# Performance work log

Hardware: AMD Instinct MI355X
Metric: run time of the kernel (lower is better)

The kernel has to match this reference:

```python
import jax, jax.numpy as jnp
import numpy as np

N_HEADS = 16

def setup_inputs() -> dict:
    key = jax.random.key(0)
    ks = jax.random.split(key, 5)
    D = 1024
    B, T = 4, 1024
    scale = 1.0 / np.sqrt(D)
    x = jax.random.normal(ks[0], (B, T, D), dtype=jnp.float32)
    Wq = jax.random.normal(ks[1], (D, D), dtype=jnp.float32) * scale
    Wk = jax.random.normal(ks[2], (D, D), dtype=jnp.float32) * scale
    Wv = jax.random.normal(ks[3], (D, D), dtype=jnp.float32) * scale
    Wo = jax.random.normal(ks[4], (D, D), dtype=jnp.float32) * scale
    return {"x": x, "Wq": Wq, "Wk": Wk, "Wv": Wv, "Wo": Wo}


def reference(x, Wq, Wk, Wv, Wo):
    # FLA BasedLinearAttention (mode='chunk', normalize=True, scale=1) with
    # Taylor feature map phi(u) = [1, u/d^{1/4}, (u (x) u)/sqrt(2 d)], so
    # phi(q)·phi(k) = 1 + s + s^2/2 where s = (q·k)/sqrt(d).
    B, T, D = x.shape
    H = N_HEADS
    d = D // H  # head_dim == feature_dim
    # torch Linear: y = x @ W.T (bias=False in FLA proj layers)
    q = (x @ Wq.T).reshape(B, T, H, d).transpose(0, 2, 1, 3)  # b h t d
    k = (x @ Wk.T).reshape(B, T, H, d).transpose(0, 2, 1, 3)
    v = (x @ Wv.T).reshape(B, T, H, d).transpose(0, 2, 1, 3)
    s = jnp.einsum('bhtd,bhsd->bhts', q, k) / jnp.sqrt(jnp.float32(d))
    scores = 1.0 + s + 0.5 * s * s  # always > 0 (= ((s+1)^2+1)/2)
    causal = jnp.tril(jnp.ones((T, T), dtype=bool))
    scores = jnp.where(causal, scores, 0.0)
    num = jnp.einsum('bhts,bhsd->bhtd', scores, v)
    den = jnp.sum(scores, axis=-1, keepdims=True)
    o = num / den  # b h t d
    o = o.transpose(0, 2, 1, 3).reshape(B, T, D)  # b t (h d)
    return o @ Wo.T
```

## Files before the change

### kernel.cpp

```cpp
#include <hip/hip_runtime.h>

typedef unsigned short u16;
typedef __attribute__((ext_vector_type(8))) short bf16x8;
typedef __attribute__((ext_vector_type(8))) unsigned short u16x8;
typedef __attribute__((ext_vector_type(4))) float f32x4;

#define MFMA16(a, b, c) __builtin_amdgcn_mfma_f32_16x16x32_bf16((a), (b), (c), 0, 0, 0)

__device__ __forceinline__ void gll16(const void* g, void* l) {
    __builtin_amdgcn_global_load_lds(
        (const __attribute__((address_space(1))) unsigned int*)g,
        (__attribute__((address_space(3))) unsigned int*)l, 16, 0, 0);
}

__device__ __forceinline__ u16 f2b(float f) {
    unsigned int u = __float_as_uint(f);
    u += 0x7fffu + ((u >> 16) & 1u);
    return (u16)(u >> 16);
}

__device__ __forceinline__ unsigned int pkcvt(float a, float b) {
    unsigned int r;
    asm("v_cvt_pk_bf16_f32 %0, %1, %2" : "=v"(r) : "v"(a), "v"(b));
    return r;
}

__global__ __launch_bounds__(256) void cast_all(const float* __restrict__ x,
                                                const float* __restrict__ w0,
                                                const float* __restrict__ w1,
                                                const float* __restrict__ w2,
                                                const float* __restrict__ w3,
                                                u16* __restrict__ xb,
                                                u16* __restrict__ wb) {
    const int bid = blockIdx.x;
    const float* s; u16* d; int off;
    if (bid < 2048) { s = x; d = xb; off = bid; }
    else {
        const int wi = (bid - 2048) >> 9;
        s = (wi == 0) ? w0 : (wi == 1) ? w1 : (wi == 2) ? w2 : w3;
        d = wb + (size_t)wi * 1048576;
        off = (bid - 2048) & 511;
    }
    const int i = (off * 256 + threadIdx.x) * 8;
    float4 a = *(const float4*)(s + i);
    float4 b = *(const float4*)(s + i + 4);
    *(uint4*)(d + i) = make_uint4(pkcvt(a.x, a.y), pkcvt(a.z, a.w),
                                  pkcvt(b.x, b.y), pkcvt(b.z, b.w));
}

template <int BM, int BN, int MODE, int SLOTS>
__global__ __launch_bounds__(256) void gemm_bt(const u16* __restrict__ A,
                                               const u16* __restrict__ W,
                                               void* __restrict__ Yv,
                                               u16* __restrict__ vT,
                                               int K, int ldY) {
    constexpr int MI = BM / 32, NJ = BN / 32;
    constexpr int ACH = BM / 16;
    constexpr int NPW = (BM + BN) / 64;
    __shared__ u16 As[2][SLOTS][BM * 32];
    __shared__ u16 Bs[2][SLOTS][BN * 32];
    const int t = threadIdx.x, w = t >> 6, lane = t & 63;
    const int quad = lane >> 4, m16 = lane & 15;
    const int wr = (w >> 1) * (BM / 2), wc = (w & 1) * (BN / 2);
    const int row0 = blockIdx.x * BM, col0 = blockIdx.y * BN;
    const int srow = lane >> 2, scol = (lane & 3) * 8;

    auto stage = [&](int buf, int slot, int k0) {
#pragma unroll
        for (int cc = 0; cc < NPW; ++cc) {
            const int c = w * NPW + cc;
            if (c < ACH)
                gll16(A + (size_t)(row0 + c * 16 + srow) * K + k0 + scol,
                      &As[buf][slot][c * 512]);
            else
                gll16(W + (size_t)(col0 + (c - ACH) * 16 + srow) * K + k0 + scol,
                      &Bs[buf][slot][(c - ACH) * 512]);
        }
    };

    f32x4 acc[MI][NJ];
#pragma unroll
    for (int i = 0; i < MI; ++i)
#pragma unroll
        for (int j = 0; j < NJ; ++j) acc[i][j] = (f32x4){0.f, 0.f, 0.f, 0.f};

    auto compute_tile = [&](int buf, int slot) {
        bf16x8 af[MI], bf[NJ];
#pragma unroll
        for (int i = 0; i < MI; ++i)
            af[i] = *(const bf16x8*)&As[buf][slot][(wr + i * 16 + m16) * 32 + quad * 8];
#pragma unroll
        for (int j = 0; j < NJ; ++j)
            bf[j] = *(const bf16x8*)&Bs[buf][slot][(wc + j * 16 + m16) * 32 + quad * 8];
#pragma unroll
        for (int i = 0; i < MI; ++i)
#pragma unroll
            for (int j = 0; j < NJ; ++j) acc[i][j] = MFMA16(af[i], bf[j], acc[i][j]);
    };

#pragma unroll
    for (int s = 0; s < SLOTS; ++s) stage(0, s, s * 32);
    const int ngroups = K / (32 * SLOTS);
    for (int g = 0; g < ngroups; ++g) {
        const int buf = g & 1;
        __syncthreads();
        const int kn = (g + 1) * SLOTS * 32;
        if (kn < K) {
#pragma unroll
            for (int s = 0; s < SLOTS; ++s) stage(buf ^ 1, s, kn + s * 32);
        }
#pragma unroll
        for (int s = 0; s < SLOTS; ++s) compute_tile(buf, s);
    }
    if constexpr (MODE == 0) {
#pragma unroll
        for (int i = 0; i < MI; ++i)
#pragma unroll
            for (int j = 0; j < NJ; ++j)
#pragma unroll
                for (int r = 0; r < 4; ++r)
                    ((float*)Yv)[(size_t)(row0 + wr + i * 16 + quad * 4 + r) * ldY +
                                 col0 + wc + j * 16 + m16] = acc[i][j][r];
    } else {
        if (col0 < 2048) {
            u16* qk = (u16*)Yv;
#pragma unroll
            for (int i = 0; i < MI; ++i)
#pragma unroll
                for (int j = 0; j < NJ; ++j)
#pragma unroll
                    for (int r = 0; r < 4; ++r)
                        qk[(size_t)(row0 + wr + i * 16 + quad * 4 + r) * 2048 +
                           col0 + wc + j * 16 + m16] = f2b(acc[i][j][r]);
        } else {
#pragma unroll
            for (int i = 0; i < MI; ++i) {
                const int rbase = row0 + wr + i * 16;
                const int bb = rbase >> 10;
                const int tok0 = (rbase & 1023) + quad * 4;
#pragma unroll
                for (int j = 0; j < NJ; ++j) {
                    const int vTrow = bb * 1024 + (col0 + wc + j * 16 + m16 - 2048);
                    *(uint2*)(vT + (size_t)vTrow * 1024 + tok0) =
                        make_uint2(pkcvt(acc[i][j][0], acc[i][j][1]),
                                   pkcvt(acc[i][j][2], acc[i][j][3]));
                }
            }
        }
    }
}

__global__ __launch_bounds__(256) void based_attn(const u16* __restrict__ qkm,
                                                  const u16* __restrict__ vT,
                                                  u16* __restrict__ o) {
    __shared__ u16 ks[2][2][64][32];
    __shared__ u16 vs[2][2][64][32];
    __shared__ u16 SsA[2][64][32];
    __shared__ u16 SsB[2][64][32];

    const int t = threadIdx.x, w = t >> 6, lane = t & 63;
    const int quad = lane >> 4, m16 = lane & 15;
    const int p = blockIdx.x, h = blockIdx.y, b = blockIdx.z;
    const int tA = p, tB = 15 - p;
    const int srow = lane >> 2, s8 = (lane & 3) * 8;
    const int qrow = w * 16 + m16;

    const size_t qbase = (size_t)b * 1024 * 2048 + h * 64;
    const size_t kbase = qbase + 1024;
    const size_t vbase = ((size_t)b * 1024 + h * 64) * 1024;

    bf16x8 qfA[2], qfB[2];
#pragma unroll
    for (int kd = 0; kd < 2; ++kd) {
        qfA[kd] = *(const bf16x8*)(qkm + qbase +
                   (size_t)(tA * 64 + qrow) * 2048 + kd * 32 + quad * 8);
        qfB[kd] = *(const bf16x8*)(qkm + qbase +
                   (size_t)(tB * 64 + qrow) * 2048 + kd * 32 + quad * 8);
    }

    auto stage_tile = [&](int kt, int buf) {
#pragma unroll
        for (int cc = 0; cc < 2; ++cc) {
            const int c = w * 2 + cc;
            const int blk = c >> 2, rc = c & 3;
            gll16(qkm + kbase + (size_t)(kt * 64 + rc * 16 + srow) * 2048 + blk * 32 + s8,
                  &ks[buf][blk][rc * 16][0]);
            gll16(vT + vbase + (size_t)(rc * 16 + srow) * 1024 + kt * 64 + blk * 32 + s8,
                  &vs[buf][blk][rc * 16][0]);
        }
    };

    bf16x8 ones;
#pragma unroll
    for (int e = 0; e < 8; ++e) ones[e] = (short)0x3F80;

    f32x4 numA[4], numB[4], denA, denB;
    denA = denB = (f32x4){0.f, 0.f, 0.f, 0.f};
#pragma unroll
    for (int j = 0; j < 4; ++j) numA[j] = numB[j] = (f32x4){0.f, 0.f, 0.f, 0.f};

    auto compute = [&](int buf, int kt) {
        const bool doA = (kt <= tA);
        f32x4 sA[4], sB[4];
#pragma unroll
        for (int jk = 0; jk < 4; ++jk)
            sA[jk] = sB[jk] = (f32x4){0.f, 0.f, 0.f, 0.f};
        __builtin_amdgcn_s_setprio(1);
#pragma unroll
        for (int kd = 0; kd < 2; ++kd)
#pragma unroll
            for (int jk = 0; jk < 4; ++jk) {
                bf16x8 af = *(const bf16x8*)&ks[buf][kd][jk * 16 + m16][quad * 8];
                sB[jk] = MFMA16(af, qfB[kd], sB[jk]);
                if (doA) sA[jk] = MFMA16(af, qfA[kd], sA[jk]);
            }
        __builtin_amdgcn_s_setprio(0);
#pragma unroll
        for (int jk = 0; jk < 4; ++jk) {
            const int kl = jk * 16 + quad * 4;
            float scB[4];
#pragma unroll
            for (int r = 0; r < 4; ++r) {
                const float u = fmaf(sB[jk][r], 0.125f, 1.0f);
                scB[r] = fmaf(u * 0.5f, u, 0.5f);
            }
            if (kt == tB) {
#pragma unroll
                for (int r = 0; r < 4; ++r)
                    if (kl + r > qrow) scB[r] = 0.f;
            }
            *(uint2*)&SsB[kl >> 5][qrow][kl & 31] =
                make_uint2(pkcvt(scB[0], scB[1]), pkcvt(scB[2], scB[3]));
            if (doA) {
                float scA[4];
#pragma unroll
                for (int r = 0; r < 4; ++r) {
                    const float u = fmaf(sA[jk][r], 0.125f, 1.0f);
                    scA[r] = fmaf(u * 0.5f, u, 0.5f);
                }
                if (kt == tA) {
#pragma unroll
                    for (int r = 0; r < 4; ++r)
                        if (kl + r > qrow) scA[r] = 0.f;
                }
                *(uint2*)&SsA[kl >> 5][qrow][kl & 31] =
                    make_uint2(pkcvt(scA[0], scA[1]), pkcvt(scA[2], scA[3]));
            }
        }
        __builtin_amdgcn_s_setprio(1);
#pragma unroll
        for (int kb = 0; kb < 2; ++kb) {
            bf16x8 vf[4];
#pragma unroll
            for (int j = 0; j < 4; ++j)
                vf[j] = *(const bf16x8*)&vs[buf][kb][j * 16 + m16][quad * 8];
            bf16x8 sfB = *(const bf16x8*)&SsB[kb][qrow][quad * 8];
#pragma unroll
            for (int j = 0; j < 4; ++j) numB[j] = MFMA16(sfB, vf[j], numB[j]);
            denB = MFMA16(sfB, ones, denB);
            if (doA) {
                bf16x8 sfA = *(const bf16x8*)&SsA[kb][qrow][quad * 8];
#pragma unroll
                for (int j = 0; j < 4; ++j) numA[j] = MFMA16(sfA, vf[j], numA[j]);
                denA = MFMA16(sfA, ones, denA);
            }
        }
        __builtin_amdgcn_s_setprio(0);
    };

    stage_tile(0, 0);
    for (int kt = 0; kt <= tB; ++kt) {
        const int buf = kt & 1;
        __syncthreads();
        if (kt + 1 <= tB) stage_tile(kt + 1, buf ^ 1);
        compute(buf, kt);
    }

#pragma unroll
    for (int r = 0; r < 4; ++r) {
        const float invA = 1.0f / denA[r], invB = 1.0f / denB[r];
        const int rowoff = w * 16 + quad * 4 + r;
        const size_t tokA = (size_t)(b * 1024 + tA * 64 + rowoff);
        const size_t tokB = (size_t)(b * 1024 + tB * 64 + rowoff);
#pragma unroll
        for (int j = 0; j < 4; ++j) {
            o[tokA * 1024 + h * 64 + j * 16 + m16] = f2b(numA[j][r] * invA);
            o[tokB * 1024 + h * 64 + j * 16 + m16] = f2b(numB[j][r] * invB);
        }
    }
}

extern "C" void kernel_launch(void* const* d_in, const int* in_sizes, int n_in,
                              void* d_out, int out_size, void* d_ws, size_t ws_size,
                              hipStream_t stream) {
    const float* x  = (const float*)d_in[0];
    const float* Wq = (const float*)d_in[1];
    const float* Wk = (const float*)d_in[2];
    const float* Wv = (const float*)d_in[3];
    const float* Wo = (const float*)d_in[4];
    float* out = (float*)d_out;

    const size_t MEL = 4096ull * 1024ull;
    u16* xb   = (u16*)d_ws;
    u16* Wqkv = xb + MEL;
    u16* Wob  = Wqkv + 3ull * 1024 * 1024;
    u16* qk   = Wob + 1024ull * 1024;
    u16* vT   = qk + 2ull * MEL;
    u16* o    = vT + MEL;

    cast_all<<<4096, 256, 0, stream>>>(x, Wq, Wk, Wv, Wo, xb, Wqkv);

    dim3 gq(32, 24);
    gemm_bt<128, 128, 1, 1><<<gq, 256, 0, stream>>>(xb, Wqkv, qk, vT, 1024, 2048);

    dim3 ga(8, 16, 4);
    based_attn<<<ga, 256, 0, stream>>>(qk, vT, o);

    dim3 go(32, 16);
    gemm_bt<128, 64, 0, 2><<<go, 256, 0, stream>>>(o, Wob, (void*)out, nullptr, 1024, 1024);
}
```

Baseline: 160.9 us.

## Rewrite attention kernel with 32x32 MFMA and register-resident score matrix

Reworks the based-attention kernel so each wave owns a 32-row query strip and uses 32x32x16 bf16 MFMAs for both QK^T and score·V. The score tile is no longer round-tripped through shared memory. It is converted to bf16 in registers and the halves are exchanged across the wave with shuffles to form the A operand. Query strips are assigned per wave in a balanced causal pattern (p, 31-p, 8+p, 23-p). Waves with shorter strips skip compute while still taking part in the shared K/V staging and barriers. This removes LDS writes and reads of the scores and lowers MFMA instruction count. The cost is more register pressure and intra-block imbalance, since the block runs to the longest strip.

New measurement: 182.3 us. 1.13x slower.

```diff
diff --git a/kernel.cpp b/kernel.cpp
--- a/kernel.cpp
+++ b/kernel.cpp
@@ -2,10 +2,11 @@
 
 typedef unsigned short u16;
 typedef __attribute__((ext_vector_type(8))) short bf16x8;
-typedef __attribute__((ext_vector_type(8))) unsigned short u16x8;
 typedef __attribute__((ext_vector_type(4))) float f32x4;
+typedef __attribute__((ext_vector_type(16))) float f32x16;
 
 #define MFMA16(a, b, c) __builtin_amdgcn_mfma_f32_16x16x32_bf16((a), (b), (c), 0, 0, 0)
+#define MFMA32(a, b, c) __builtin_amdgcn_mfma_f32_32x32x16_bf16((a), (b), (c), 0, 0, 0)
 
 __device__ __forceinline__ void gll16(const void* g, void* l) {
     __builtin_amdgcn_global_load_lds(
@@ -150,33 +151,29 @@
     }
 }
 
-__global__ __launch_bounds__(256) void based_attn(const u16* __restrict__ qkm,
-                                                  const u16* __restrict__ vT,
-                                                  u16* __restrict__ o) {
+__global__ __launch_bounds__(256) void based_attn32(const u16* __restrict__ qkm,
+                                                    const u16* __restrict__ vT,
+                                                    u16* __restrict__ o) {
     __shared__ u16 ks[2][2][64][32];
     __shared__ u16 vs[2][2][64][32];
-    __shared__ u16 SsA[2][64][32];
-    __shared__ u16 SsB[2][64][32];
 
     const int t = threadIdx.x, w = t >> 6, lane = t & 63;
-    const int quad = lane >> 4, m16 = lane & 15;
-    const int p = blockIdx.x, h = blockIdx.y, b = blockIdx.z;
-    const int tA = p, tB = 15 - p;
+    const int m = lane & 31, h = lane >> 5;
+    const int p = blockIdx.x, hh = blockIdx.y, b = blockIdx.z;
+    const int j = (w == 0) ? p : (w == 1) ? (31 - p) : (w == 2) ? (8 + p) : (23 - p);
+    const int ktmax_w = j >> 1;
+    const int KTMAX = (31 - p) >> 1;
     const int srow = lane >> 2, s8 = (lane & 3) * 8;
-    const int qrow = w * 16 + m16;
-
-    const size_t qbase = (size_t)b * 1024 * 2048 + h * 64;
+
+    const size_t qbase = (size_t)b * 1024 * 2048 + hh * 64;
     const size_t kbase = qbase + 1024;
-    const size_t vbase = ((size_t)b * 1024 + h * 64) * 1024;
-
-    bf16x8 qfA[2], qfB[2];
-#pragma unroll
-    for (int kd = 0; kd < 2; ++kd) {
-        qfA[kd] = *(const bf16x8*)(qkm + qbase +
-                   (size_t)(tA * 64 + qrow) * 2048 + kd * 32 + quad * 8);
-        qfB[kd] = *(const bf16x8*)(qkm + qbase +
-                   (size_t)(tB * 64 + qrow) * 2048 + kd * 32 + quad * 8);
-    }
+    const size_t vbase = ((size_t)b * 1024 + hh * 64) * 1024;
+
+    bf16x8 qf[4];
+#pragma unroll
+    for (int kd = 0; kd < 4; ++kd)
+        qf[kd] = *(const bf16x8*)(qkm + qbase + (size_t)(j * 32 + m) * 2048 +
+                                  kd * 16 + h * 8);
 
     auto stage_tile = [&](int kt, int buf) {
 #pragma unroll
@@ -194,99 +191,95 @@
 #pragma unroll
     for (int e = 0; e < 8; ++e) ones[e] = (short)0x3F80;
 
-    f32x4 numA[4], numB[4], denA, denB;
-    denA = denB = (f32x4){0.f, 0.f, 0.f, 0.f};
-#pragma unroll
-    for (int j = 0; j < 4; ++j) numA[j] = numB[j] = (f32x4){0.f, 0.f, 0.f, 0.f};
+    f32x16 num0, num1, den;
+#pragma unroll
+    for (int e = 0; e < 16; ++e) { num0[e] = 0.f; num1[e] = 0.f; den[e] = 0.f; }
 
     auto compute = [&](int buf, int kt) {
-        const bool doA = (kt <= tA);
-        f32x4 sA[4], sB[4];
-#pragma unroll
-        for (int jk = 0; jk < 4; ++jk)
-            sA[jk] = sB[jk] = (f32x4){0.f, 0.f, 0.f, 0.f};
-        __builtin_amdgcn_s_setprio(1);
-#pragma unroll
-        for (int kd = 0; kd < 2; ++kd)
-#pragma unroll
-            for (int jk = 0; jk < 4; ++jk) {
-                bf16x8 af = *(const bf16x8*)&ks[buf][kd][jk * 16 + m16][quad * 8];
-                sB[jk] = MFMA16(af, qfB[kd], sB[jk]);
-                if (doA) sA[jk] = MFMA16(af, qfA[kd], sA[jk]);
+        const bool diag = (kt == ktmax_w);
+        const bool odd = (j & 1) != 0;
+        const bool do1 = (!diag) || odd;
+
+        f32x16 s0, s1;
+#pragma unroll
+        for (int e = 0; e < 16; ++e) { s0[e] = 0.f; s1[e] = 0.f; }
+#pragma unroll
+        for (int kd = 0; kd < 4; ++kd) {
+            bf16x8 k0 = *(const bf16x8*)&ks[buf][kd >> 1][m][(kd & 1) * 16 + h * 8];
+            s0 = MFMA32(k0, qf[kd], s0);
+            if (do1) {
+                bf16x8 k1 = *(const bf16x8*)&ks[buf][kd >> 1][32 + m][(kd & 1) * 16 + h * 8];
+                s1 = MFMA32(k1, qf[kd], s1);
             }
-        __builtin_amdgcn_s_setprio(0);
-#pragma unroll
-        for (int jk = 0; jk < 4; ++jk) {
-            const int kl = jk * 16 + quad * 4;
-            float scB[4];
-#pragma unroll
-            for (int r = 0; r < 4; ++r) {
-                const float u = fmaf(sB[jk][r], 0.125f, 1.0f);
-                scB[r] = fmaf(u * 0.5f, u, 0.5f);
+        }
+
+        float sc0[16], sc1[16];
+#pragma unroll
+        for (int r = 0; r < 16; ++r) {
+            const int kl = (r & 3) + 8 * (r >> 2) + 4 * h;
+            float u0 = fmaf(s0[r], 0.125f, 1.0f);
+            float v0 = fmaf(u0 * 0.5f, u0, 0.5f);
+            if (diag && !odd && kl > m) v0 = 0.f;
+            sc0[r] = v0;
+            float v1 = 0.f;
+            if (do1) {
+                float u1 = fmaf(s1[r], 0.125f, 1.0f);
+                v1 = fmaf(u1 * 0.5f, u1, 0.5f);
+                if (diag && odd && kl > m) v1 = 0.f;
             }
-            if (kt == tB) {
-#pragma unroll
-                for (int r = 0; r < 4; ++r)
-                    if (kl + r > qrow) scB[r] = 0.f;
+            sc1[r] = v1;
+        }
+
+        unsigned o0[8], o1[8], p0[8], p1[8];
+#pragma unroll
+        for (int i = 0; i < 8; ++i) {
+            o0[i] = pkcvt(sc0[2 * i], sc0[2 * i + 1]);
+            o1[i] = pkcvt(sc1[2 * i], sc1[2 * i + 1]);
+        }
+#pragma unroll
+        for (int i = 0; i < 8; ++i) {
+            p0[i] = __shfl_xor(o0[i], 32);
+            p1[i] = __shfl_xor(o1[i], 32);
+        }
+
+#pragma unroll
+        for (int ksi = 0; ksi < 4; ++ksi) {
+            const int bx = (ksi & 1) * 4 + 2 * h;
+            union { unsigned u[4]; bf16x8 v; } af;
+            if (ksi < 2) {
+                af.u[0] = h ? p0[bx] : o0[bx];
+                af.u[1] = h ? p0[bx + 1] : o0[bx + 1];
+                af.u[2] = h ? o0[bx] : p0[bx];
+                af.u[3] = h ? o0[bx + 1] : p0[bx + 1];
+            } else {
+                af.u[0] = h ? p1[bx] : o1[bx];
+                af.u[1] = h ? p1[bx + 1] : o1[bx + 1];
+                af.u[2] = h ? o1[bx] : p1[bx];
+                af.u[3] = h ? o1[bx + 1] : p1[bx + 1];
             }
-            *(uint2*)&SsB[kl >> 5][qrow][kl & 31] =
-                make_uint2(pkcvt(scB[0], scB[1]), pkcvt(scB[2], scB[3]));
-            if (doA) {
-                float scA[4];
-#pragma unroll
-                for (int r = 0; r < 4; ++r) {
-                    const float u = fmaf(sA[jk][r], 0.125f, 1.0f);
-                    scA[r] = fmaf(u * 0.5f, u, 0.5f);
-                }
-                if (kt == tA) {
-#pragma unroll
-                    for (int r = 0; r < 4; ++r)
-                        if (kl + r > qrow) scA[r] = 0.f;
-                }
-                *(uint2*)&SsA[kl >> 5][qrow][kl & 31] =
-                    make_uint2(pkcvt(scA[0], scA[1]), pkcvt(scA[2], scA[3]));
-            }
-        }
-        __builtin_amdgcn_s_setprio(1);
-#pragma unroll
-        for (int kb = 0; kb < 2; ++kb) {
-            bf16x8 vf[4];
-#pragma unroll
-            for (int j = 0; j < 4; ++j)
-                vf[j] = *(const bf16x8*)&vs[buf][kb][j * 16 + m16][quad * 8];
-            bf16x8 sfB = *(const bf16x8*)&SsB[kb][qrow][quad * 8];
-#pragma unroll
-            for (int j = 0; j < 4; ++j) numB[j] = MFMA16(sfB, vf[j], numB[j]);
-            denB = MFMA16(sfB, ones, denB);
-            if (doA) {
-                bf16x8 sfA = *(const bf16x8*)&SsA[kb][qrow][quad * 8];
-#pragma unroll
-                for (int j = 0; j < 4; ++j) numA[j] = MFMA16(sfA, vf[j], numA[j]);
-                denA = MFMA16(sfA, ones, denA);
-            }
-        }
-        __builtin_amdgcn_s_setprio(0);
+            bf16x8 v0 = *(const bf16x8*)&vs[buf][ksi >> 1][m][(ksi & 1) * 16 + h * 8];
+            bf16x8 v1 = *(const bf16x8*)&vs[buf][ksi >> 1][32 + m][(ksi & 1) * 16 + h * 8];
+            num0 = MFMA32(af.v, v0, num0);
+            num1 = MFMA32(af.v, v1, num1);
+            den  = MFMA32(af.v, ones, den);
+        }
     };
 
     stage_tile(0, 0);
-    for (int kt = 0; kt <= tB; ++kt) {
+    for (int kt = 0; kt <= KTMAX; ++kt) {
         const int buf = kt & 1;
         __syncthreads();
-        if (kt + 1 <= tB) stage_tile(kt + 1, buf ^ 1);
-        compute(buf, kt);
-    }
-
-#pragma unroll
-    for (int r = 0; r < 4; ++r) {
-        const float invA = 1.0f / denA[r], invB = 1.0f / denB[r];
-        const int rowoff = w * 16 + quad * 4 + r;
-        const size_t tokA = (size_t)(b * 1024 + tA * 64 + rowoff);
-        const size_t tokB = (size_t)(b * 1024 + tB * 64 + rowoff);
-#pragma unroll
-        for (int j = 0; j < 4; ++j) {
-            o[tokA * 1024 + h * 64 + j * 16 + m16] = f2b(numA[j][r] * invA);
-            o[tokB * 1024 + h * 64 + j * 16 + m16] = f2b(numB[j][r] * invB);
-        }
+        if (kt < KTMAX) stage_tile(kt + 1, buf ^ 1);
+        if (kt <= ktmax_w) compute(buf, kt);
+    }
+
+#pragma unroll
+    for (int r = 0; r < 16; ++r) {
+        const int q = (r & 3) + 8 * (r >> 2) + 4 * h;
+        const float inv = 1.0f / den[r];
+        const size_t tok = (size_t)(b * 1024 + j * 32 + q);
+        o[tok * 1024 + hh * 64 + m]      = f2b(num0[r] * inv);
+        o[tok * 1024 + hh * 64 + 32 + m] = f2b(num1[r] * inv);
     }
 }
 
@@ -314,7 +307,7 @@
     gemm_bt<128, 128, 1, 1><<<gq, 256, 0, stream>>>(xb, Wqkv, qk, vT, 1024, 2048);
 
     dim3 ga(8, 16, 4);
-    based_attn<<<ga, 256, 0, stream>>>(qk, vT, o);
+    based_attn32<<<ga, 256, 0, stream>>>(qk, vT, o);
 
     dim3 go(32, 16);
     gemm_bt<128, 64, 0, 2><<<go, 256, 0, stream>>>(o, Wob, (void*)out, nullptr, 1024, 1024);
```

## Keep attention scores in registers and use one query tile per block

Applied to the files above, without the earlier changes.

The attention kernel no longer writes the score tile to shared memory and reads it back. It computes S transposed (K·Q), packs the scores into bf16 register fragments, and feeds them straight into 16x16x16 MFMAs against V read from LDS. The denominator becomes a scalar row sum with a cross-lane shuffle instead of an extra MFMA against a ones vector. The grid goes from paired query tiles (p, 15-p) per block to one query tile per block, which doubles the block count but loses the pairing's load balance and its sharing of K/V staging between two tiles.

Result: slower. 204.6 us (+27.2%).

```diff
diff --git a/kernel.cpp b/kernel.cpp
--- a/kernel.cpp
+++ b/kernel.cpp
@@ -2,10 +2,20 @@
 
 typedef unsigned short u16;
 typedef __attribute__((ext_vector_type(8))) short bf16x8;
-typedef __attribute__((ext_vector_type(8))) unsigned short u16x8;
+typedef __attribute__((ext_vector_type(4))) short s16x4;
+typedef __attribute__((ext_vector_type(2))) int i32x2;
 typedef __attribute__((ext_vector_type(4))) float f32x4;
 
 #define MFMA16(a, b, c) __builtin_amdgcn_mfma_f32_16x16x32_bf16((a), (b), (c), 0, 0, 0)
+
+__device__ __forceinline__ void mfma161616(i32x2 a, i32x2 b, f32x4& c) {
+#if __has_builtin(__builtin_amdgcn_mfma_f32_16x16x16bf16_1k)
+    union { i32x2 i; s16x4 s; } ua{a}, ub{b};
+    c = __builtin_amdgcn_mfma_f32_16x16x16bf16_1k(ua.s, ub.s, c, 0, 0, 0);
+#else
+    asm("v_mfma_f32_16x16x16_bf16 %0, %1, %2, %0" : "+v"(c) : "v"(a), "v"(b));
+#endif
+}
 
 __device__ __forceinline__ void gll16(const void* g, void* l) {
     __builtin_amdgcn_global_load_lds(
@@ -155,13 +165,10 @@
                                                   u16* __restrict__ o) {
     __shared__ u16 ks[2][2][64][32];
     __shared__ u16 vs[2][2][64][32];
-    __shared__ u16 SsA[2][64][32];
-    __shared__ u16 SsB[2][64][32];
 
     const int t = threadIdx.x, w = t >> 6, lane = t & 63;
     const int quad = lane >> 4, m16 = lane & 15;
-    const int p = blockIdx.x, h = blockIdx.y, b = blockIdx.z;
-    const int tA = p, tB = 15 - p;
+    const int tq = blockIdx.x, h = blockIdx.y, b = blockIdx.z;
     const int srow = lane >> 2, s8 = (lane & 3) * 8;
     const int qrow = w * 16 + m16;
 
@@ -169,14 +176,11 @@
     const size_t kbase = qbase + 1024;
     const size_t vbase = ((size_t)b * 1024 + h * 64) * 1024;
 
-    bf16x8 qfA[2], qfB[2];
-#pragma unroll
-    for (int kd = 0; kd < 2; ++kd) {
-        qfA[kd] = *(const bf16x8*)(qkm + qbase +
-                   (size_t)(tA * 64 + qrow) * 2048 + kd * 32 + quad * 8);
-        qfB[kd] = *(const bf16x8*)(qkm + qbase +
-                   (size_t)(tB * 64 + qrow) * 2048 + kd * 32 + quad * 8);
-    }
+    bf16x8 qf[2];
+#pragma unroll
+    for (int kd = 0; kd < 2; ++kd)
+        qf[kd] = *(const bf16x8*)(qkm + qbase +
+                  (size_t)(tq * 64 + qrow) * 2048 + kd * 32 + quad * 8);
 
     auto stage_tile = [&](int kt, int buf) {
 #pragma unroll
@@ -190,104 +194,72 @@
         }
     };
 
-    bf16x8 ones;
-#pragma unroll
-    for (int e = 0; e < 8; ++e) ones[e] = (short)0x3F80;
-
-    f32x4 numA[4], numB[4], denA, denB;
-    denA = denB = (f32x4){0.f, 0.f, 0.f, 0.f};
-#pragma unroll
-    for (int j = 0; j < 4; ++j) numA[j] = numB[j] = (f32x4){0.f, 0.f, 0.f, 0.f};
+    f32x4 num[4];
+    float dens = 0.f;
+#pragma unroll
+    for (int j = 0; j < 4; ++j) num[j] = (f32x4){0.f, 0.f, 0.f, 0.f};
 
     auto compute = [&](int buf, int kt) {
-        const bool doA = (kt <= tA);
-        f32x4 sA[4], sB[4];
-#pragma unroll
-        for (int jk = 0; jk < 4; ++jk)
-            sA[jk] = sB[jk] = (f32x4){0.f, 0.f, 0.f, 0.f};
+        f32x4 s[4];
+#pragma unroll
+        for (int jk = 0; jk < 4; ++jk) s[jk] = (f32x4){0.f, 0.f, 0.f, 0.f};
         __builtin_amdgcn_s_setprio(1);
 #pragma unroll
         for (int kd = 0; kd < 2; ++kd)
 #pragma unroll
             for (int jk = 0; jk < 4; ++jk) {
                 bf16x8 af = *(const bf16x8*)&ks[buf][kd][jk * 16 + m16][quad * 8];
-                sB[jk] = MFMA16(af, qfB[kd], sB[jk]);
-                if (doA) sA[jk] = MFMA16(af, qfA[kd], sA[jk]);
+                s[jk] = MFMA16(af, qf[kd], s[jk]);
             }
         __builtin_amdgcn_s_setprio(0);
+        i32x2 sb[4];
 #pragma unroll
         for (int jk = 0; jk < 4; ++jk) {
             const int kl = jk * 16 + quad * 4;
-            float scB[4];
+            float sc[4];
 #pragma unroll
             for (int r = 0; r < 4; ++r) {
-                const float u = fmaf(sB[jk][r], 0.125f, 1.0f);
-                scB[r] = fmaf(u * 0.5f, u, 0.5f);
-            }
-            if (kt == tB) {
+                const float u = fmaf(s[jk][r], 0.125f, 1.0f);
+                sc[r] = fmaf(u * 0.5f, u, 0.5f);
+            }
+            if (kt == tq) {
 #pragma unroll
                 for (int r = 0; r < 4; ++r)
-                    if (kl + r > qrow) scB[r] = 0.f;
-            }
-            *(uint2*)&SsB[kl >> 5][qrow][kl & 31] =
-                make_uint2(pkcvt(scB[0], scB[1]), pkcvt(scB[2], scB[3]));
-            if (doA) {
-                float scA[4];
-#pragma unroll
-                for (int r = 0; r < 4; ++r) {
-                    const float u = fmaf(sA[jk][r], 0.125f, 1.0f);
-                    scA[r] = fmaf(u * 0.5f, u, 0.5f);
-                }
-                if (kt == tA) {
-#pragma unroll
-                    for (int r = 0; r < 4; ++r)
-                        if (kl + r > qrow) scA[r] = 0.f;
-                }
-                *(uint2*)&SsA[kl >> 5][qrow][kl & 31] =
-                    make_uint2(pkcvt(scA[0], scA[1]), pkcvt(scA[2], scA[3]));
-            }
+                    if (kl + r > qrow) sc[r] = 0.f;
+            }
+            dens += sc[0] + sc[1] + sc[2] + sc[3];
+            sb[jk][0] = (int)pkcvt(sc[0], sc[1]);
+            sb[jk][1] = (int)pkcvt(sc[2], sc[3]);
         }
         __builtin_amdgcn_s_setprio(1);
 #pragma unroll
-        for (int kb = 0; kb < 2; ++kb) {
-            bf16x8 vf[4];
-#pragma unroll
-            for (int j = 0; j < 4; ++j)
-                vf[j] = *(const bf16x8*)&vs[buf][kb][j * 16 + m16][quad * 8];
-            bf16x8 sfB = *(const bf16x8*)&SsB[kb][qrow][quad * 8];
-#pragma unroll
-            for (int j = 0; j < 4; ++j) numB[j] = MFMA16(sfB, vf[j], numB[j]);
-            denB = MFMA16(sfB, ones, denB);
-            if (doA) {
-                bf16x8 sfA = *(const bf16x8*)&SsA[kb][qrow][quad * 8];
-#pragma unroll
-                for (int j = 0; j < 4; ++j) numA[j] = MFMA16(sfA, vf[j], numA[j]);
-                denA = MFMA16(sfA, ones, denA);
+        for (int jk = 0; jk < 4; ++jk) {
+            const int kb = jk >> 1, ko = (jk & 1) * 16 + quad * 4;
+#pragma unroll
+            for (int j = 0; j < 4; ++j) {
+                i32x2 va = *(const i32x2*)&vs[buf][kb][j * 16 + m16][ko];
+                mfma161616(va, sb[jk], num[j]);
             }
         }
         __builtin_amdgcn_s_setprio(0);
     };
 
     stage_tile(0, 0);
-    for (int kt = 0; kt <= tB; ++kt) {
+    for (int kt = 0; kt <= tq; ++kt) {
         const int buf = kt & 1;
         __syncthreads();
-        if (kt + 1 <= tB) stage_tile(kt + 1, buf ^ 1);
+        if (kt < tq) stage_tile(kt + 1, buf ^ 1);
         compute(buf, kt);
     }
 
-#pragma unroll
-    for (int r = 0; r < 4; ++r) {
-        const float invA = 1.0f / denA[r], invB = 1.0f / denB[r];
-        const int rowoff = w * 16 + quad * 4 + r;
-        const size_t tokA = (size_t)(b * 1024 + tA * 64 + rowoff);
-        const size_t tokB = (size_t)(b * 1024 + tB * 64 + rowoff);
-#pragma unroll
-        for (int j = 0; j < 4; ++j) {
-            o[tokA * 1024 + h * 64 + j * 16 + m16] = f2b(numA[j][r] * invA);
-            o[tokB * 1024 + h * 64 + j * 16 + m16] = f2b(numB[j][r] * invB);
-        }
-    }
+    dens += __shfl_xor(dens, 16); dens += __shfl_xor(dens, 32);
+    const float inv = 1.0f / dens;
+    const size_t tok = (size_t)(b * 1024 + tq * 64 + qrow);
+#pragma unroll
+    for (int j = 0; j < 4; ++j)
+        *(uint2*)(o + tok * 1024 + h * 64 + j * 16 + quad * 4) =
+            make_uint2(pkcvt(num[j][0] * inv, num[j][1] * inv),
+                       pkcvt(num[j][2] * inv, num[j][3] * inv));
 }
 
 extern "C" void kernel_launch(void* const* d_in, const int* in_sizes, int n_in,
@@ -313,7 +285,7 @@
     dim3 gq(32, 24);
     gemm_bt<128, 128, 1, 1><<<gq, 256, 0, stream>>>(xb, Wqkv, qk, vT, 1024, 2048);
 
-    dim3 ga(8, 16, 4);
+    dim3 ga(16, 16, 4);
     based_attn<<<ga, 256, 0, stream>>>(qk, vT, o);
 
     dim3 go(32, 16);
```
